# Kernel tuning notes

Measured on AMD Instinct MI355X. Metric: run time of the kernel, lower is better.

The kernel has to match this reference:

```python
import jax, jax.numpy as jnp
import numpy as np

B = 131072
D_IN = 385          # 384-d embedding + 1 correctness feature
D_H = 192           # both trunk layers resolve to max(.,192)=192 per source
Q = 1000            # number of questions
C = 16              # classes per head (uniform padding of per-question heads)


def setup_inputs() -> dict:
    key = jax.random.key(0)
    ks = jax.random.split(key, 9)
    x = jax.random.normal(ks[0], (B, D_IN), dtype=jnp.float32)
    question_ids = jax.random.randint(ks[1], (B,), 0, Q, dtype=jnp.int32)
    is_correct = jax.random.randint(ks[2], (B,), 0, 2, dtype=jnp.int32)
    W1 = jax.random.normal(ks[3], (D_IN, D_H), dtype=jnp.float32) * 0.05
    b1 = jnp.zeros((D_H,), dtype=jnp.float32)
    W2 = jax.random.normal(ks[4], (D_H, D_H), dtype=jnp.float32) * 0.05
    b2 = jnp.zeros((D_H,), dtype=jnp.float32)
    # Head bank: slots [0,Q) = false heads, [Q,2Q) = true heads.
    W_heads = jax.random.normal(ks[5], (2 * Q, C, D_H), dtype=jnp.float32) * 0.05
    b_heads = jax.random.normal(ks[6], (2 * Q, C), dtype=jnp.float32) * 0.05
    return {"x": x, "question_ids": question_ids, "is_correct": is_correct,
            "W1": W1, "b1": b1, "W2": W2, "b2": b2,
            "W_heads": W_heads, "b_heads": b_heads}


def reference(x, question_ids, is_correct, W1, b1, W2, b2, W_heads, b_heads):
    # Shared trunk (eval mode: dropout = identity)
    h = jax.nn.relu(x @ W1 + b1)            # [B, 192]
    feat = jax.nn.relu(h @ W2 + b2)         # [B, 192]
    # Hard routing: pick true or false head for this question.
    Qn = W_heads.shape[0] // 2
    idx = question_ids + is_correct * Qn    # [B]
    Wq = W_heads[idx]                       # [B, C, 192] gather (memory-bound)
    bq = b_heads[idx]                       # [B, C]
    logits = jnp.einsum('bcd,bd->bc', Wq, feat) + bq  # per-sample routed linear
    return logits
```

## Files before the change

kernel.cpp:

```cpp
#include <hip/hip_runtime.h>
#include <stdint.h>
#include <stddef.h>


typedef short s8v __attribute__((ext_vector_type(8)));
typedef float f4v __attribute__((ext_vector_type(4)));
typedef float f4a __attribute__((ext_vector_type(4), aligned(4)));

namespace {
constexpr int kDin = 385;
constexpr int kDh  = 192;
constexpr int kQ   = 1000;
constexpr int kC   = 16;
constexpr int kH   = 2 * kQ;
constexpr int BM   = 64;
constexpr int NT   = 256;
constexpr int NK1  = 13;
constexpr int NK2  = 6;
constexpr int CHUNK = 12 * 64 * 8;
constexpr int H2   = 200;

constexpr size_t WS_W1   = 0;
constexpr size_t WS_W2   = 163840;
constexpr size_t WS_HIST = 245760;
constexpr size_t WS_CUR  = 253952;
constexpr size_t WS_PERM = 262144;
}

__device__ __forceinline__ unsigned short f2bf(float f) {
  unsigned int u = __float_as_uint(f);
  u = u + 0x7fffu + ((u >> 16) & 1u);
  return (unsigned short)(u >> 16);
}
__device__ __forceinline__ float bf2f(short h) {
  return __uint_as_float(((unsigned int)(unsigned short)h) << 16);
}

__global__ void zero_hist(int* hist) {
  int i = blockIdx.x * blockDim.x + threadIdx.x;
  if (i < 2048) hist[i] = 0;
}
__global__ void hist_k(const int* __restrict__ qid, const int* __restrict__ isc,
                       int B, int* __restrict__ hist) {
  int i = blockIdx.x * blockDim.x + threadIdx.x;
  if (i < B) atomicAdd(&hist[qid[i] + isc[i] * kQ], 1);
}
__global__ void scan_k(const int* __restrict__ hist, int* __restrict__ cursor) {
  __shared__ int s[2048];
  int t = threadIdx.x;
  s[t] = hist[t]; s[t + 1024] = hist[t + 1024];
  __syncthreads();
  for (int d = 1; d < 2048; d <<= 1) {
    int a0 = (t >= d) ? s[t - d] : 0;
    int a1 = (t + 1024 >= d) ? s[t + 1024 - d] : 0;
    __syncthreads();
    s[t] += a0; s[t + 1024] += a1;
    __syncthreads();
  }
  cursor[t] = s[t] - hist[t];
  cursor[t + 1024] = s[t + 1024] - hist[t + 1024];
}
__global__ void scatter_k(const int* __restrict__ qid, const int* __restrict__ isc,
                          int B, int* __restrict__ cursor, int* __restrict__ perm) {
  int i = blockIdx.x * blockDim.x + threadIdx.x;
  if (i < B) {
    int h = qid[i] + isc[i] * kQ;
    int pos = atomicAdd(&cursor[h], 1);
    perm[pos] = i;
  }
}

__global__ void prep_swizzle(const float* __restrict__ W, int K, int NKS,
                             unsigned short* __restrict__ out) {
  int idx = blockIdx.x * blockDim.x + threadIdx.x;
  int total = NKS * CHUNK;
  if (idx >= total) return;
  int j  = idx & 7;
  int l  = (idx >> 3) & 63;
  int rem = idx % CHUNK;
  int t  = rem >> 9;
  int kk = idx / CHUNK;
  int k  = kk * 32 + ((l >> 4) << 3) + j;
  int c  = t * 16 + (l & 15);
  float v = (k < K) ? W[(size_t)k * kDh + c] : 0.f;
  out[idx] = f2bf(v);
}

__global__ __launch_bounds__(NT, 4)
void fused_qmlp3(const float* __restrict__ x,
                 const int*   __restrict__ qid,
                 const int*   __restrict__ isc,
                 const float* __restrict__ b1,
                 const float* __restrict__ b2,
                 const float* __restrict__ Wh,
                 const float* __restrict__ bh,
                 const unsigned short* __restrict__ W1sw,
                 const unsigned short* __restrict__ W2sw,
                 const int*   __restrict__ perm,
                 float* __restrict__ out) {
  __shared__ __align__(16) unsigned short hS[BM * H2];
  __shared__ __align__(16) unsigned short bS[CHUNK];
  __shared__ int permS[BM];
  __shared__ int idxS[BM];

  const int tid  = threadIdx.x;
  const int lane = tid & 63, wid = tid >> 6;
  const int m = lane & 15, quad = lane >> 4;
  const int rh = wid & 1, ch = wid >> 1;
  const int row0 = blockIdx.x * BM;

  if (tid < BM) {
    int p = perm[row0 + tid];
    permS[tid] = p;
    idxS[tid] = qid[p] + isc[p] * kQ;
  }
  __syncthreads();

  const size_t xr0 = (size_t)permS[rh * 32 + m] * kDin;
  const size_t xr1 = (size_t)permS[rh * 32 + m + 16] * kDin;

  f4v acc0[6], acc1[6];
  #pragma unroll
  for (int t = 0; t < 6; ++t) {
    acc0[t] = (f4v){0.f, 0.f, 0.f, 0.f};
    acc1[t] = (f4v){0.f, 0.f, 0.f, 0.f};
  }

  for (int kk = 0; kk < NK1; ++kk) {
    const s8v* src = (const s8v*)(W1sw + (size_t)kk * CHUNK);
    s8v w0 = src[tid], w1 = src[tid + NT], w2 = src[tid + 2 * NT];

    s8v a0, a1;
    if (kk < NK1 - 1) {
      const float* p0 = x + xr0 + kk * 32 + quad * 8;
      const float* p1 = x + xr1 + kk * 32 + quad * 8;
      f4a v00 = *(const f4a*)p0, v01 = *(const f4a*)(p0 + 4);
      f4a v10 = *(const f4a*)p1, v11 = *(const f4a*)(p1 + 4);
      #pragma unroll
      for (int j = 0; j < 4; ++j) {
        a0[j]     = (short)f2bf(v00[j]);
        a0[j + 4] = (short)f2bf(v01[j]);
        a1[j]     = (short)f2bf(v10[j]);
        a1[j + 4] = (short)f2bf(v11[j]);
      }
    } else {
      float v0 = (quad == 0) ? x[xr0 + 384] : 0.f;
      float v1 = (quad == 0) ? x[xr1 + 384] : 0.f;
      a0 = (s8v){0,0,0,0,0,0,0,0};
      a1 = (s8v){0,0,0,0,0,0,0,0};
      a0[0] = (short)f2bf(v0);
      a1[0] = (short)f2bf(v1);
    }

    ((s8v*)bS)[tid] = w0;
    ((s8v*)bS)[tid + NT] = w1;
    ((s8v*)bS)[tid + 2 * NT] = w2;
    __syncthreads();

    #pragma unroll
    for (int t = 0; t < 6; ++t) {
      s8v b = *(const s8v*)&bS[((ch * 6 + t) * 64 + lane) * 8];
      acc0[t] = __builtin_amdgcn_mfma_f32_16x16x32_bf16(a0, b, acc0[t], 0, 0, 0);
      acc1[t] = __builtin_amdgcn_mfma_f32_16x16x32_bf16(a1, b, acc1[t], 0, 0, 0);
    }
    __syncthreads();
  }

  #pragma unroll
  for (int t = 0; t < 6; ++t) {
    int c = ch * 96 + t * 16 + m;
    float bb = b1[c];
    #pragma unroll
    for (int r4 = 0; r4 < 4; ++r4) {
      int r = rh * 32 + quad * 4 + r4;
      float v0 = acc0[t][r4] + bb; v0 = v0 > 0.f ? v0 : 0.f;
      hS[r * H2 + c] = f2bf(v0);
      float v1 = acc1[t][r4] + bb; v1 = v1 > 0.f ? v1 : 0.f;
      hS[(r + 16) * H2 + c] = f2bf(v1);
      acc0[t][r4] = 0.f;
      acc1[t][r4] = 0.f;
    }
  }

  const int ar0 = (rh * 32 + m) * H2;
  for (int kk = 0; kk < NK2; ++kk) {
    const s8v* src = (const s8v*)(W2sw + (size_t)kk * CHUNK);
    s8v w0 = src[tid], w1 = src[tid + NT], w2 = src[tid + 2 * NT];
    ((s8v*)bS)[tid] = w0;
    ((s8v*)bS)[tid + NT] = w1;
    ((s8v*)bS)[tid + 2 * NT] = w2;
    __syncthreads();

    s8v a0 = *(const s8v*)&hS[ar0 + kk * 32 + quad * 8];
    s8v a1 = *(const s8v*)&hS[ar0 + 16 * H2 + kk * 32 + quad * 8];
    #pragma unroll
    for (int t = 0; t < 6; ++t) {
      s8v b = *(const s8v*)&bS[((ch * 6 + t) * 64 + lane) * 8];
      acc0[t] = __builtin_amdgcn_mfma_f32_16x16x32_bf16(a0, b, acc0[t], 0, 0, 0);
      acc1[t] = __builtin_amdgcn_mfma_f32_16x16x32_bf16(a1, b, acc1[t], 0, 0, 0);
    }
    __syncthreads();
  }

  #pragma unroll
  for (int t = 0; t < 6; ++t) {
    int c = ch * 96 + t * 16 + m;
    float bb = b2[c];
    #pragma unroll
    for (int r4 = 0; r4 < 4; ++r4) {
      int r = rh * 32 + quad * 4 + r4;
      float v0 = acc0[t][r4] + bb;
      hS[r * H2 + c] = f2bf(v0 > 0.f ? v0 : 0.f);
      float v1 = acc1[t][r4] + bb;
      hS[(r + 16) * H2 + c] = f2bf(v1 > 0.f ? v1 : 0.f);
    }
  }
  __syncthreads();

  const int cls = lane >> 2, qp = lane & 3;
  #pragma unroll 2
  for (int rr = 0; rr < 16; ++rr) {
    int row = wid * 16 + rr;
    int hidx = idxS[row];
    int g = permS[row];
    const float4* wp = (const float4*)(Wh + ((size_t)hidx * kC + cls) * kDh + qp * 48);
    const unsigned short* fr = &hS[row * H2 + qp * 48];
    float s = 0.f;
    #pragma unroll
    for (int t = 0; t < 6; ++t) {
      s8v f8 = *(const s8v*)&fr[t * 8];
      float4 wA = wp[2 * t], wB = wp[2 * t + 1];
      s += wA.x * bf2f(f8[0]) + wA.y * bf2f(f8[1]) +
           wA.z * bf2f(f8[2]) + wA.w * bf2f(f8[3]);
      s += wB.x * bf2f(f8[4]) + wB.y * bf2f(f8[5]) +
           wB.z * bf2f(f8[6]) + wB.w * bf2f(f8[7]);
    }
    s += __shfl_xor(s, 1);
    s += __shfl_xor(s, 2);
    if (qp == 0)
      out[(size_t)g * kC + cls] = s + bh[(size_t)hidx * kC + cls];
  }
}

extern "C" void kernel_launch(void* const* d_in, const int* in_sizes, int n_in,
                              void* d_out, int out_size, void* d_ws, size_t ws_size,
                              hipStream_t stream) {
  const float* x  = (const float*)d_in[0];
  const int*   qd = (const int*)  d_in[1];
  const int*   ic = (const int*)  d_in[2];
  const float* W1 = (const float*)d_in[3];
  const float* b1 = (const float*)d_in[4];
  const float* W2 = (const float*)d_in[5];
  const float* b2 = (const float*)d_in[6];
  const float* Wh = (const float*)d_in[7];
  const float* bh = (const float*)d_in[8];
  float* out = (float*)d_out;

  char* ws = (char*)d_ws;
  unsigned short* W1sw = (unsigned short*)(ws + WS_W1);
  unsigned short* W2sw = (unsigned short*)(ws + WS_W2);
  int* hist   = (int*)(ws + WS_HIST);
  int* cursor = (int*)(ws + WS_CUR);
  int* perm   = (int*)(ws + WS_PERM);

  int B = in_sizes[1];

  zero_hist<<<2, 1024, 0, stream>>>(hist);
  hist_k<<<(B + 255) / 256, 256, 0, stream>>>(qd, ic, B, hist);
  scan_k<<<1, 1024, 0, stream>>>(hist, cursor);
  scatter_k<<<(B + 255) / 256, 256, 0, stream>>>(qd, ic, B, cursor, perm);

  prep_swizzle<<<(NK1 * CHUNK + 255) / 256, 256, 0, stream>>>(W1, kDin, NK1, W1sw);
  prep_swizzle<<<(NK2 * CHUNK + 255) / 256, 256, 0, stream>>>(W2, kDh,  NK2, W2sw);

  fused_qmlp3<<<B / BM, NT, 0, stream>>>(x, qd, ic, b1, b2, Wh, bh,
                                         W1sw, W2sw, perm, out);
}
```

Baseline: 476.1 us.

## Software-pipeline x and weight loads in trunk GEMMs and merge prep kernels

```diff
diff --git a/kernel.cpp b/kernel.cpp
--- a/kernel.cpp
+++ b/kernel.cpp
@@ -12,7 +12,6 @@
 constexpr int kDh  = 192;
 constexpr int kQ   = 1000;
 constexpr int kC   = 16;
-constexpr int kH   = 2 * kQ;
 constexpr int BM   = 64;
 constexpr int NT   = 256;
 constexpr int NK1  = 13;
@@ -36,45 +35,8 @@
   return __uint_as_float(((unsigned int)(unsigned short)h) << 16);
 }
 
-__global__ void zero_hist(int* hist) {
-  int i = blockIdx.x * blockDim.x + threadIdx.x;
-  if (i < 2048) hist[i] = 0;
-}
-__global__ void hist_k(const int* __restrict__ qid, const int* __restrict__ isc,
-                       int B, int* __restrict__ hist) {
-  int i = blockIdx.x * blockDim.x + threadIdx.x;
-  if (i < B) atomicAdd(&hist[qid[i] + isc[i] * kQ], 1);
-}
-__global__ void scan_k(const int* __restrict__ hist, int* __restrict__ cursor) {
-  __shared__ int s[2048];
-  int t = threadIdx.x;
-  s[t] = hist[t]; s[t + 1024] = hist[t + 1024];
-  __syncthreads();
-  for (int d = 1; d < 2048; d <<= 1) {
-    int a0 = (t >= d) ? s[t - d] : 0;
-    int a1 = (t + 1024 >= d) ? s[t + 1024 - d] : 0;
-    __syncthreads();
-    s[t] += a0; s[t + 1024] += a1;
-    __syncthreads();
-  }
-  cursor[t] = s[t] - hist[t];
-  cursor[t + 1024] = s[t + 1024] - hist[t + 1024];
-}
-__global__ void scatter_k(const int* __restrict__ qid, const int* __restrict__ isc,
-                          int B, int* __restrict__ cursor, int* __restrict__ perm) {
-  int i = blockIdx.x * blockDim.x + threadIdx.x;
-  if (i < B) {
-    int h = qid[i] + isc[i] * kQ;
-    int pos = atomicAdd(&cursor[h], 1);
-    perm[pos] = i;
-  }
-}
-
-__global__ void prep_swizzle(const float* __restrict__ W, int K, int NKS,
-                             unsigned short* __restrict__ out) {
-  int idx = blockIdx.x * blockDim.x + threadIdx.x;
-  int total = NKS * CHUNK;
-  if (idx >= total) return;
+__device__ __forceinline__ void swz_one(const float* W, int K, int idx,
+                                        unsigned short* out) {
   int j  = idx & 7;
   int l  = (idx >> 3) & 63;
   int rem = idx % CHUNK;
@@ -86,8 +48,51 @@
   out[idx] = f2bf(v);
 }
 
+__global__ void combo_prep(const int* __restrict__ qid, const int* __restrict__ isc,
+                           int B, int nbH,
+                           const float* __restrict__ W1, const float* __restrict__ W2,
+                           int* __restrict__ hist,
+                           unsigned short* __restrict__ W1sw,
+                           unsigned short* __restrict__ W2sw) {
+  int bid = blockIdx.x;
+  if (bid < nbH) {
+    int i = bid * 256 + threadIdx.x;
+    if (i < B) atomicAdd(&hist[qid[i] + isc[i] * kQ], 1);
+  } else if (bid < nbH + 312) {
+    swz_one(W1, kDin, (bid - nbH) * 256 + threadIdx.x, W1sw);
+  } else {
+    swz_one(W2, kDh, (bid - nbH - 312) * 256 + threadIdx.x, W2sw);
+  }
+}
+
+__global__ void scan_k(const int* __restrict__ hist, int* __restrict__ cursor) {
+  __shared__ int s[2048];
+  int t = threadIdx.x;
+  s[t] = hist[t]; s[t + 1024] = hist[t + 1024];
+  __syncthreads();
+  for (int d = 1; d < 2048; d <<= 1) {
+    int a0 = (t >= d) ? s[t - d] : 0;
+    int a1 = (t + 1024 >= d) ? s[t + 1024 - d] : 0;
+    __syncthreads();
+    s[t] += a0; s[t + 1024] += a1;
+    __syncthreads();
+  }
+  cursor[t] = s[t] - hist[t];
+  cursor[t + 1024] = s[t + 1024] - hist[t + 1024];
+}
+
+__global__ void scatter_k(const int* __restrict__ qid, const int* __restrict__ isc,
+                          int B, int* __restrict__ cursor, int* __restrict__ perm) {
+  int i = blockIdx.x * blockDim.x + threadIdx.x;
+  if (i < B) {
+    int h = qid[i] + isc[i] * kQ;
+    int pos = atomicAdd(&cursor[h], 1);
+    perm[pos] = i;
+  }
+}
+
 __global__ __launch_bounds__(NT, 4)
-void fused_qmlp3(const float* __restrict__ x,
+void fused_qmlp4(const float* __restrict__ x,
                  const int*   __restrict__ qid,
                  const int*   __restrict__ isc,
                  const float* __restrict__ b1,
@@ -114,6 +119,13 @@
     permS[tid] = p;
     idxS[tid] = qid[p] + isc[p] * kQ;
   }
+
+  float bb1[6], bb2[6];
+  #pragma unroll
+  for (int t = 0; t < 6; ++t) {
+    bb1[t] = b1[ch * 96 + t * 16 + m];
+    bb2[t] = b2[ch * 96 + t * 16 + m];
+  }
   __syncthreads();
 
   const size_t xr0 = (size_t)permS[rh * 32 + m] * kDin;
@@ -126,37 +138,59 @@
     acc1[t] = (f4v){0.f, 0.f, 0.f, 0.f};
   }
 
-  for (int kk = 0; kk < NK1; ++kk) {
-    const s8v* src = (const s8v*)(W1sw + (size_t)kk * CHUNK);
-    s8v w0 = src[tid], w1 = src[tid + NT], w2 = src[tid + 2 * NT];
-
-    s8v a0, a1;
+  f4a xb[2][4];
+  s8v wb[2][3];
+
+  auto LDX = [&](int kk, f4a* dst) {
     if (kk < NK1 - 1) {
       const float* p0 = x + xr0 + kk * 32 + quad * 8;
       const float* p1 = x + xr1 + kk * 32 + quad * 8;
-      f4a v00 = *(const f4a*)p0, v01 = *(const f4a*)(p0 + 4);
-      f4a v10 = *(const f4a*)p1, v11 = *(const f4a*)(p1 + 4);
-      #pragma unroll
-      for (int j = 0; j < 4; ++j) {
-        a0[j]     = (short)f2bf(v00[j]);
-        a0[j + 4] = (short)f2bf(v01[j]);
-        a1[j]     = (short)f2bf(v10[j]);
-        a1[j + 4] = (short)f2bf(v11[j]);
-      }
+      dst[0] = *(const f4a*)p0;
+      dst[1] = *(const f4a*)(p0 + 4);
+      dst[2] = *(const f4a*)p1;
+      dst[3] = *(const f4a*)(p1 + 4);
     } else {
       float v0 = (quad == 0) ? x[xr0 + 384] : 0.f;
       float v1 = (quad == 0) ? x[xr1 + 384] : 0.f;
-      a0 = (s8v){0,0,0,0,0,0,0,0};
-      a1 = (s8v){0,0,0,0,0,0,0,0};
-      a0[0] = (short)f2bf(v0);
-      a1[0] = (short)f2bf(v1);
-    }
-
-    ((s8v*)bS)[tid] = w0;
-    ((s8v*)bS)[tid + NT] = w1;
-    ((s8v*)bS)[tid + 2 * NT] = w2;
-    __syncthreads();
-
+      dst[0] = (f4a){v0, 0.f, 0.f, 0.f};
+      dst[1] = (f4a){0.f, 0.f, 0.f, 0.f};
+      dst[2] = (f4a){v1, 0.f, 0.f, 0.f};
+      dst[3] = (f4a){0.f, 0.f, 0.f, 0.f};
+    }
+  };
+  auto LDW1 = [&](int kk, s8v* dst) {
+    const s8v* s_ = (const s8v*)(W1sw + (size_t)kk * CHUNK);
+    dst[0] = s_[tid]; dst[1] = s_[tid + NT]; dst[2] = s_[tid + 2 * NT];
+  };
+  auto LDW2 = [&](int kk, s8v* dst) {
+    const s8v* s_ = (const s8v*)(W2sw + (size_t)kk * CHUNK);
+    dst[0] = s_[tid]; dst[1] = s_[tid + NT]; dst[2] = s_[tid + 2 * NT];
+  };
+
+  LDX(0, xb[0]);
+  LDW1(0, wb[0]);
+  LDX(1, xb[1]);
+
+  #pragma unroll
+  for (int kk = 0; kk < NK1; ++kk) {
+    const int cur = kk & 1, nxt = cur ^ 1;
+    if (kk + 1 < NK1) LDW1(kk + 1, wb[nxt]);
+
+    ((s8v*)bS)[tid] = wb[cur][0];
+    ((s8v*)bS)[tid + NT] = wb[cur][1];
+    ((s8v*)bS)[tid + 2 * NT] = wb[cur][2];
+
+    s8v a0, a1;
+    #pragma unroll
+    for (int j = 0; j < 4; ++j) {
+      a0[j]     = (short)f2bf(xb[cur][0][j]);
+      a0[j + 4] = (short)f2bf(xb[cur][1][j]);
+      a1[j]     = (short)f2bf(xb[cur][2][j]);
+      a1[j + 4] = (short)f2bf(xb[cur][3][j]);
+    }
+    if (kk + 2 < NK1) LDX(kk + 2, xb[cur]);
+
+    __syncthreads();
     #pragma unroll
     for (int t = 0; t < 6; ++t) {
       s8v b = *(const s8v*)&bS[((ch * 6 + t) * 64 + lane) * 8];
@@ -169,13 +203,12 @@
   #pragma unroll
   for (int t = 0; t < 6; ++t) {
     int c = ch * 96 + t * 16 + m;
-    float bb = b1[c];
     #pragma unroll
     for (int r4 = 0; r4 < 4; ++r4) {
       int r = rh * 32 + quad * 4 + r4;
-      float v0 = acc0[t][r4] + bb; v0 = v0 > 0.f ? v0 : 0.f;
+      float v0 = acc0[t][r4] + bb1[t]; v0 = v0 > 0.f ? v0 : 0.f;
       hS[r * H2 + c] = f2bf(v0);
-      float v1 = acc1[t][r4] + bb; v1 = v1 > 0.f ? v1 : 0.f;
+      float v1 = acc1[t][r4] + bb1[t]; v1 = v1 > 0.f ? v1 : 0.f;
       hS[(r + 16) * H2 + c] = f2bf(v1);
       acc0[t][r4] = 0.f;
       acc1[t][r4] = 0.f;
@@ -183,12 +216,15 @@
   }
 
   const int ar0 = (rh * 32 + m) * H2;
+  LDW2(0, wb[0]);
+  #pragma unroll
   for (int kk = 0; kk < NK2; ++kk) {
-    const s8v* src = (const s8v*)(W2sw + (size_t)kk * CHUNK);
-    s8v w0 = src[tid], w1 = src[tid + NT], w2 = src[tid + 2 * NT];
-    ((s8v*)bS)[tid] = w0;
-    ((s8v*)bS)[tid + NT] = w1;
-    ((s8v*)bS)[tid + 2 * NT] = w2;
+    const int cur = kk & 1, nxt = cur ^ 1;
+    if (kk + 1 < NK2) LDW2(kk + 1, wb[nxt]);
+
+    ((s8v*)bS)[tid] = wb[cur][0];
+    ((s8v*)bS)[tid + NT] = wb[cur][1];
+    ((s8v*)bS)[tid + 2 * NT] = wb[cur][2];
     __syncthreads();
 
     s8v a0 = *(const s8v*)&hS[ar0 + kk * 32 + quad * 8];
@@ -205,13 +241,12 @@
   #pragma unroll
   for (int t = 0; t < 6; ++t) {
     int c = ch * 96 + t * 16 + m;
-    float bb = b2[c];
     #pragma unroll
     for (int r4 = 0; r4 < 4; ++r4) {
       int r = rh * 32 + quad * 4 + r4;
-      float v0 = acc0[t][r4] + bb;
+      float v0 = acc0[t][r4] + bb2[t];
       hS[r * H2 + c] = f2bf(v0 > 0.f ? v0 : 0.f);
-      float v1 = acc1[t][r4] + bb;
+      float v1 = acc1[t][r4] + bb2[t];
       hS[(r + 16) * H2 + c] = f2bf(v1 > 0.f ? v1 : 0.f);
     }
   }
@@ -264,15 +299,14 @@
   int* perm   = (int*)(ws + WS_PERM);
 
   int B = in_sizes[1];
-
-  zero_hist<<<2, 1024, 0, stream>>>(hist);
-  hist_k<<<(B + 255) / 256, 256, 0, stream>>>(qd, ic, B, hist);
+  int nbH = (B + 255) / 256;
+
+  hipMemsetAsync(hist, 0, 2048 * sizeof(int), stream);
+  combo_prep<<<nbH + 312 + 144, 256, 0, stream>>>(qd, ic, B, nbH, W1, W2,
+                                                  hist, W1sw, W2sw);
   scan_k<<<1, 1024, 0, stream>>>(hist, cursor);
   scatter_k<<<(B + 255) / 256, 256, 0, stream>>>(qd, ic, B, cursor, perm);
 
-  prep_swizzle<<<(NK1 * CHUNK + 255) / 256, 256, 0, stream>>>(W1, kDin, NK1, W1sw);
-  prep_swizzle<<<(NK2 * CHUNK + 255) / 256, 256, 0, stream>>>(W2, kDh,  NK2, W2sw);
-
-  fused_qmlp3<<<B / BM, NT, 0, stream>>>(x, qd, ic, b1, b2, Wh, bh,
+  fused_qmlp4<<<B / BM, NT, 0, stream>>>(x, qd, ic, b1, b2, Wh, bh,
                                          W1sw, W2sw, perm, out);
 }
```

Measured after the change: 504.1 us. 1.06x slower.

## Compute routed head logits with MFMA per head group and merge prep kernels

Applied to the files above, without the earlier changes.

```diff
diff --git a/kernel.cpp b/kernel.cpp
--- a/kernel.cpp
+++ b/kernel.cpp
@@ -12,7 +12,6 @@
 constexpr int kDh  = 192;
 constexpr int kQ   = 1000;
 constexpr int kC   = 16;
-constexpr int kH   = 2 * kQ;
 constexpr int BM   = 64;
 constexpr int NT   = 256;
 constexpr int NK1  = 13;
@@ -32,19 +31,34 @@
   u = u + 0x7fffu + ((u >> 16) & 1u);
   return (unsigned short)(u >> 16);
 }
-__device__ __forceinline__ float bf2f(short h) {
-  return __uint_as_float(((unsigned int)(unsigned short)h) << 16);
-}
-
-__global__ void zero_hist(int* hist) {
-  int i = blockIdx.x * blockDim.x + threadIdx.x;
-  if (i < 2048) hist[i] = 0;
-}
-__global__ void hist_k(const int* __restrict__ qid, const int* __restrict__ isc,
-                       int B, int* __restrict__ hist) {
-  int i = blockIdx.x * blockDim.x + threadIdx.x;
-  if (i < B) atomicAdd(&hist[qid[i] + isc[i] * kQ], 1);
-}
+
+__device__ __forceinline__ void swz_one(const float* W, int K, int i,
+                                        unsigned short* out) {
+  int k = i / kDh;
+  int c = i - k * kDh;
+  float v = (k < K) ? W[(size_t)k * kDh + c] : 0.f;
+  int oi = (k >> 5) * CHUNK + (((c >> 4) * 64 + ((k >> 3) & 3) * 16 + (c & 15)) << 3)
+         + (k & 7);
+  out[oi] = f2bf(v);
+}
+
+__global__ void combo_prep(const int* __restrict__ qid, const int* __restrict__ isc,
+                           int B, int nbH,
+                           const float* __restrict__ W1, const float* __restrict__ W2,
+                           int* __restrict__ hist,
+                           unsigned short* __restrict__ W1sw,
+                           unsigned short* __restrict__ W2sw) {
+  int bid = blockIdx.x;
+  if (bid < nbH) {
+    int i = bid * 256 + threadIdx.x;
+    if (i < B) atomicAdd(&hist[qid[i] + isc[i] * kQ], 1);
+  } else if (bid < nbH + 312) {
+    swz_one(W1, kDin, (bid - nbH) * 256 + threadIdx.x, W1sw);
+  } else {
+    swz_one(W2, kDh, (bid - nbH - 312) * 256 + threadIdx.x, W2sw);
+  }
+}
+
 __global__ void scan_k(const int* __restrict__ hist, int* __restrict__ cursor) {
   __shared__ int s[2048];
   int t = threadIdx.x;
@@ -60,6 +74,7 @@
   cursor[t] = s[t] - hist[t];
   cursor[t + 1024] = s[t + 1024] - hist[t + 1024];
 }
+
 __global__ void scatter_k(const int* __restrict__ qid, const int* __restrict__ isc,
                           int B, int* __restrict__ cursor, int* __restrict__ perm) {
   int i = blockIdx.x * blockDim.x + threadIdx.x;
@@ -70,24 +85,8 @@
   }
 }
 
-__global__ void prep_swizzle(const float* __restrict__ W, int K, int NKS,
-                             unsigned short* __restrict__ out) {
-  int idx = blockIdx.x * blockDim.x + threadIdx.x;
-  int total = NKS * CHUNK;
-  if (idx >= total) return;
-  int j  = idx & 7;
-  int l  = (idx >> 3) & 63;
-  int rem = idx % CHUNK;
-  int t  = rem >> 9;
-  int kk = idx / CHUNK;
-  int k  = kk * 32 + ((l >> 4) << 3) + j;
-  int c  = t * 16 + (l & 15);
-  float v = (k < K) ? W[(size_t)k * kDh + c] : 0.f;
-  out[idx] = f2bf(v);
-}
-
 __global__ __launch_bounds__(NT, 4)
-void fused_qmlp3(const float* __restrict__ x,
+void fused_qmlp5(const float* __restrict__ x,
                  const int*   __restrict__ qid,
                  const int*   __restrict__ isc,
                  const float* __restrict__ b1,
@@ -217,28 +216,41 @@
   }
   __syncthreads();
 
-  const int cls = lane >> 2, qp = lane & 3;
-  #pragma unroll 2
-  for (int rr = 0; rr < 16; ++rr) {
-    int row = wid * 16 + rr;
-    int hidx = idxS[row];
-    int g = permS[row];
-    const float4* wp = (const float4*)(Wh + ((size_t)hidx * kC + cls) * kDh + qp * 48);
-    const unsigned short* fr = &hS[row * H2 + qp * 48];
-    float s = 0.f;
-    #pragma unroll
-    for (int t = 0; t < 6; ++t) {
-      s8v f8 = *(const s8v*)&fr[t * 8];
-      float4 wA = wp[2 * t], wB = wp[2 * t + 1];
-      s += wA.x * bf2f(f8[0]) + wA.y * bf2f(f8[1]) +
-           wA.z * bf2f(f8[2]) + wA.w * bf2f(f8[3]);
-      s += wB.x * bf2f(f8[4]) + wB.y * bf2f(f8[5]) +
-           wB.z * bf2f(f8[6]) + wB.w * bf2f(f8[7]);
-    }
-    s += __shfl_xor(s, 1);
-    s += __shfl_xor(s, 2);
-    if (qp == 0)
-      out[(size_t)g * kC + cls] = s + bh[(size_t)hidx * kC + cls];
+  {
+    const int w16 = wid * 16;
+    const int hm = idxS[w16 + m];
+    unsigned rem = 0xFFFFu;
+    while (rem) {
+      int r0 = (int)__builtin_ctz(rem);
+      int h = idxS[w16 + r0];
+      unsigned long long bal = __ballot(hm == h);
+      unsigned mask16 = (unsigned)(bal & 0xFFFFu);
+      rem &= ~mask16;
+      bool valid = (hm == h);
+
+      const float* wq = Wh + ((size_t)h * kC + m) * kDh + quad * 8;
+      f4v acc = (f4v){0.f, 0.f, 0.f, 0.f};
+      #pragma unroll
+      for (int kk = 0; kk < 6; ++kk) {
+        float4 wlo = *(const float4*)(wq + kk * 32);
+        float4 whi = *(const float4*)(wq + kk * 32 + 4);
+        s8v bfr;
+        bfr[0] = (short)f2bf(wlo.x); bfr[1] = (short)f2bf(wlo.y);
+        bfr[2] = (short)f2bf(wlo.z); bfr[3] = (short)f2bf(wlo.w);
+        bfr[4] = (short)f2bf(whi.x); bfr[5] = (short)f2bf(whi.y);
+        bfr[6] = (short)f2bf(whi.z); bfr[7] = (short)f2bf(whi.w);
+        s8v afr = *(const s8v*)&hS[(w16 + m) * H2 + kk * 32 + quad * 8];
+        if (!valid) afr = (s8v){0,0,0,0,0,0,0,0};
+        acc = __builtin_amdgcn_mfma_f32_16x16x32_bf16(afr, bfr, acc, 0, 0, 0);
+      }
+      float bhv = bh[(size_t)h * kC + m];
+      #pragma unroll
+      for (int reg = 0; reg < 4; ++reg) {
+        int r = quad * 4 + reg;
+        if ((mask16 >> r) & 1u)
+          out[(size_t)permS[w16 + r] * kC + m] = acc[reg] + bhv;
+      }
+    }
   }
 }
 
@@ -264,15 +276,14 @@
   int* perm   = (int*)(ws + WS_PERM);
 
   int B = in_sizes[1];
-
-  zero_hist<<<2, 1024, 0, stream>>>(hist);
-  hist_k<<<(B + 255) / 256, 256, 0, stream>>>(qd, ic, B, hist);
+  int nbH = (B + 255) / 256;
+
+  hipMemsetAsync(hist, 0, 2048 * sizeof(int), stream);
+  combo_prep<<<nbH + 312 + 144, 256, 0, stream>>>(qd, ic, B, nbH, W1, W2,
+                                                  hist, W1sw, W2sw);
   scan_k<<<1, 1024, 0, stream>>>(hist, cursor);
   scatter_k<<<(B + 255) / 256, 256, 0, stream>>>(qd, ic, B, cursor, perm);
 
-  prep_swizzle<<<(NK1 * CHUNK + 255) / 256, 256, 0, stream>>>(W1, kDin, NK1, W1sw);
-  prep_swizzle<<<(NK2 * CHUNK + 255) / 256, 256, 0, stream>>>(W2, kDh,  NK2, W2sw);
-
-  fused_qmlp3<<<B / BM, NT, 0, stream>>>(x, qd, ic, b1, b2, Wh, bh,
+  fused_qmlp5<<<B / BM, NT, 0, stream>>>(x, qd, ic, b1, b2, Wh, bh,
                                          W1sw, W2sw, perm, out);
 }
```

New measurement: 398.2 us. 16.4% less time.
